# Kernel optimization log

Hardware: AMD Instinct MI355X
Metric: run time of the kernel (lower is better)

Reference implementation:

```python
import jax, jax.numpy as jnp
import numpy as np

K = 20.0          # wavenumber_k
L = 0.01          # grid_spacing_l
_lm = [L ** (i + 1) for i in range(7)]
C1 = jnp.array([[_lm[0], _lm[1]/2, _lm[2]/3, _lm[3]/4],
                [_lm[1]/2, _lm[2]/3, _lm[3]/4, _lm[4]/5],
                [_lm[2]/3, _lm[3]/4, _lm[4]/5, _lm[5]/6],
                [_lm[3]/4, _lm[4]/5, _lm[5]/6, _lm[6]/7]], dtype=jnp.float32)
C2 = jnp.array([[0,0,0,0],[0,0,0,0],[0,0,4*_lm[0],6*_lm[1]],[0,0,6*_lm[1],12*_lm[2]]], dtype=jnp.float32)
C3 = jnp.array([[0,0,0,0],[0,0,0,0],[2*_lm[0],_lm[1],2/3*_lm[2],1/2*_lm[3]],[3*_lm[1],2*_lm[2],3/2*_lm[3],6/5*_lm[4]]], dtype=jnp.float32)
M  = jnp.array([[1,0,0,0],[0,0,1,0],[-3/_lm[1],3/_lm[1],-2/_lm[0],-1/_lm[0]],[2/_lm[2],-2/_lm[2],1/_lm[1],1/_lm[1]]], dtype=jnp.float32)


def setup_inputs() -> dict:
    key = jax.random.key(0)
    x = jax.random.normal(key, (16, 4, 512, 512), dtype=jnp.float32)
    return {"x": x}


def _helmholtz(x):
    # corner views: (B, 4, H-1, W-1)
    tl = x[:, :, :-1, :-1]
    tr = x[:, :, :-1, 1:]
    bl = x[:, :, 1:, :-1]
    br = x[:, :, 1:, 1:]
    # rows replicate the original module exactly (including row_3's use of
    # du_xy_tl twice and du_x_tr); row_4 stacked on last dim.
    row1 = jnp.stack([tl[:, 0], tr[:, 0], tl[:, 2], tr[:, 2]], axis=-1)
    row2 = jnp.stack([bl[:, 0], br[:, 0], bl[:, 2], br[:, 2]], axis=-1)
    row3 = jnp.stack([tl[:, 3], tr[:, 1], tl[:, 3], tr[:, 3]], axis=-1)
    row4 = jnp.stack([bl[:, 1], br[:, 1], bl[:, 3], br[:, 3]], axis=-1)
    Q = jnp.stack([row1, row2, row3, row4], axis=-2)  # (B, H-1, W-1, 4, 4)
    # A = M @ Q @ M^T
    A = jnp.einsum('ij,bhwjk,lk->bhwil', M, Q, M)

    def quad(Cm):
        # sum over all entries of A @ Cm @ A^T, per patch -> (B, H-1, W-1)
        return jnp.einsum('bhwij,jk,bhwlk->bhw', A, Cm, A)

    s1 = jnp.sum(C1)
    s2 = jnp.sum(C2)
    s3 = jnp.sum(C3)
    qC1  = quad(C1)
    qC2  = quad(C2)
    qC3T = quad(C3.T)
    qC3  = quad(C3)
    k2 = K * K
    patch = (s2 * qC1 + s1 * qC2 + (k2 * k2) * s1 * qC1
             + 2.0 * s3 * qC3T + 2.0 * k2 * s1 * qC3 + 2.0 * k2 * s3 * qC1)
    return jnp.mean(patch)


def reference(x):
    return _helmholtz(x)
```

## Files before the change

kernel.cpp:

```cpp
#include <hip/hip_runtime.h>


struct HParams {
    float u0, u1, u2, u3;
    float H00, H11, H22, H33;
    float H01_2, H02_2, H03_2, H12_2, H13_2, H23_2;
};

#define BSIZE 256

__device__ __forceinline__ float f4get(const float4& v, int k) {
    switch (k & 3) { case 0: return v.x; case 1: return v.y; case 2: return v.z; default: return v.w; }
}

struct Fields { float f1[8], f2[8], f3[8], f4[8], f5[8]; };

#define LOADROW(B, r) do {                                                  \
    _Pragma("unroll")                                                       \
    for (int ch = 0; ch < 4; ++ch) {                                        \
        const size_t base_ = (size_t)ch * 65536u + (size_t)(r) * 128u + cq; \
        B[2*ch]   = px[base_];                                              \
        B[2*ch+1] = px[base_ + 1];                                          \
    } } while (0)

#define FIELDS(F, B) do {                                                   \
    _Pragma("unroll")                                                       \
    for (int j = 0; j < 8; ++j) {                                           \
        const float x0_ = f4get(B[0 + (j>>2)], j);                          \
        const float x1_ = f4get(B[2 + (j>>2)], j);                          \
        const float x2_ = f4get(B[4 + (j>>2)], j);                          \
        const float x3_ = f4get(B[6 + (j>>2)], j);                          \
        const float t0_ = P.u0 * x0_;                                       \
        F.f1[j] = fmaf(P.u2, x3_, t0_);                                     \
        F.f2[j] = fmaf(P.u2, x1_, t0_);                                     \
        F.f3[j] = fmaf(P.u3, x1_, P.u1 * x0_);                              \
        F.f4[j] = fmaf(P.u2, x3_, P.u0 * x2_);                              \
        F.f5[j] = fmaf(P.u3, x3_, P.u1 * x2_);                              \
    } } while (0)

#define PATCH(Ft, Fb) do {                                                  \
    float aV[8], bV[8], cV[8];                                              \
    _Pragma("unroll")                                                       \
    for (int j = 0; j < 8; ++j) {                                           \
        aV[j] = Ft.f1[j] + Fb.f3[j];                                        \
        bV[j] = Ft.f2[j] + Fb.f3[j];                                        \
        cV[j] = Ft.f4[j] + Fb.f5[j];                                        \
    }                                                                       \
    const float bn_ = __shfl_down(bV[0], 1, 64);                            \
    const float cn_ = __shfl_down(cV[0], 1, 64);                            \
    float rowsum_ = 0.0f;                                                   \
    _Pragma("unroll")                                                       \
    for (int j = 0; j < 8; ++j) {                                           \
        const float w0_ = aV[j];                                            \
        const float w1_ = (j < 7) ? bV[j+1] : bn_;                          \
        const float w2_ = cV[j];                                            \
        const float w3_ = (j < 7) ? cV[j+1] : cn_;                          \
        const float q0_ = fmaf(P.H03_2, w3_, fmaf(P.H02_2, w2_, fmaf(P.H01_2, w1_, P.H00 * w0_))); \
        const float q1_ = fmaf(P.H13_2, w3_, fmaf(P.H12_2, w2_, P.H11 * w1_)); \
        const float q2_ = fmaf(P.H23_2, w3_, P.H22 * w2_);                  \
        const float q3_ = P.H33 * w3_;                                      \
        const float pq_ = fmaf(w0_, q0_, fmaf(w1_, q1_, fmaf(w2_, q2_, w3_ * q3_))); \
        if (j < 7 || lane < 63) rowsum_ += pq_;                             \
    }                                                                       \
    acc += (double)rowsum_;                                                 \
} while (0)

__global__ __launch_bounds__(BSIZE) void helm_main(const float* __restrict__ x,
                                                   double* __restrict__ partial,
                                                   HParams P)
{
    const int t    = threadIdx.x;
    const int lane = t & 63;
    const int wid  = t >> 6;
    const int sid  = blockIdx.x * 4 + wid;
    const int b    = sid >> 6;
    const int tile = sid & 63;
    const int h0   = tile * 8;
    const int hend = min(h0 + 8, 511);

    const float4* px = (const float4*)(x + (size_t)b * (4u * 512u * 512u));
    const int cq = lane * 2;

    float4 A0[8], A1[8];
    Fields Fa, Fb;
    double acc = 0.0;

    LOADROW(A0, h0);
    LOADROW(A1, h0 + 1);
    FIELDS(Fa, A0);

    int r = h0 + 1;
    while (true) {
        if (r + 1 <= hend) LOADROW(A0, r + 1);
        FIELDS(Fb, A1);
        PATCH(Fa, Fb);
        ++r; if (r > hend) break;
        if (r + 1 <= hend) LOADROW(A1, r + 1);
        FIELDS(Fa, A0);
        PATCH(Fb, Fa);
        ++r; if (r > hend) break;
    }

    #pragma unroll
    for (int off = 32; off > 0; off >>= 1)
        acc += __shfl_down(acc, off, 64);
    if (lane == 0) partial[sid] = acc;
}

__global__ __launch_bounds__(BSIZE) void helm_reduce(const double* __restrict__ partial,
                                                     float* __restrict__ out, int n)
{
    __shared__ double wsum[4];
    const int t = threadIdx.x;
    double a = 0.0;
    for (int i = t; i < n; i += BSIZE) a += partial[i];
    #pragma unroll
    for (int off = 32; off > 0; off >>= 1)
        a += __shfl_down(a, off, 64);
    if ((t & 63) == 0) wsum[t >> 6] = a;
    __syncthreads();
    if (t == 0) {
        const double sum = wsum[0] + wsum[1] + wsum[2] + wsum[3];
        out[0] = (float)(sum / (16.0 * 511.0 * 511.0));
    }
}

extern "C" void kernel_launch(void* const* d_in, const int* in_sizes, int n_in,
                              void* d_out, int out_size, void* d_ws, size_t ws_size,
                              hipStream_t stream) {
    const float* x  = (const float*)d_in[0];
    float* out      = (float*)d_out;
    double* partial = (double*)d_ws;

    const double L = 0.01;
    double lm[7];
    lm[0] = L;
    for (int i = 1; i < 7; ++i) lm[i] = lm[i - 1] * L;

    double C1[4][4], C2[4][4] = {}, C3[4][4] = {};
    for (int i = 0; i < 4; ++i)
        for (int j = 0; j < 4; ++j)
            C1[i][j] = lm[i + j] / (double)(i + j + 1);
    C2[2][2] = 4.0 * lm[0];  C2[2][3] = 6.0 * lm[1];
    C2[3][2] = 6.0 * lm[1];  C2[3][3] = 12.0 * lm[2];
    C3[2][0] = 2.0 * lm[0];  C3[2][1] = lm[1];
    C3[2][2] = (2.0 / 3.0) * lm[2];  C3[2][3] = 0.5 * lm[3];
    C3[3][0] = 3.0 * lm[1];  C3[3][1] = 2.0 * lm[2];
    C3[3][2] = 1.5 * lm[3];  C3[3][3] = (6.0 / 5.0) * lm[4];

    const double M[4][4] = {
        {1.0, 0.0, 0.0, 0.0},
        {0.0, 0.0, 1.0, 0.0},
        {-3.0 / lm[1], 3.0 / lm[1], -2.0 / lm[0], -1.0 / lm[0]},
        { 2.0 / lm[2], -2.0 / lm[2], 1.0 / lm[1],  1.0 / lm[1]}
    };

    double s1 = 0.0, s2 = 0.0, s3 = 0.0;
    for (int i = 0; i < 4; ++i)
        for (int j = 0; j < 4; ++j) {
            s1 += C1[i][j]; s2 += C2[i][j]; s3 += C3[i][j];
        }

    const double k2 = 20.0 * 20.0;
    const double a1 = s2 + k2 * k2 * s1 + 2.0 * k2 * s3;
    const double a2 = s1;
    const double a3 = 2.0 * s3 + 2.0 * k2 * s1;

    double G[4][4];
    for (int i = 0; i < 4; ++i)
        for (int j = 0; j < 4; ++j)
            G[i][j] = a1 * C1[i][j] + a2 * C2[i][j] + a3 * C3[i][j];

    double H[4][4] = {};
    for (int jj = 0; jj < 4; ++jj)
        for (int kk = 0; kk < 4; ++kk) {
            double s = 0.0;
            for (int a = 0; a < 4; ++a)
                for (int bb = 0; bb < 4; ++bb)
                    s += M[a][jj] * G[a][bb] * M[bb][kk];
            H[jj][kk] = s;
        }
    double Hs[4][4];
    for (int i = 0; i < 4; ++i)
        for (int j = 0; j < 4; ++j)
            Hs[i][j] = 0.5 * (H[i][j] + H[j][i]);

    double u[4];
    for (int j = 0; j < 4; ++j)
        u[j] = M[0][j] + M[1][j] + M[2][j] + M[3][j];

    HParams P;
    P.u0 = (float)u[0]; P.u1 = (float)u[1]; P.u2 = (float)u[2]; P.u3 = (float)u[3];
    P.H00 = (float)Hs[0][0]; P.H11 = (float)Hs[1][1];
    P.H22 = (float)Hs[2][2]; P.H33 = (float)Hs[3][3];
    P.H01_2 = (float)(2.0 * Hs[0][1]); P.H02_2 = (float)(2.0 * Hs[0][2]);
    P.H03_2 = (float)(2.0 * Hs[0][3]); P.H12_2 = (float)(2.0 * Hs[1][2]);
    P.H13_2 = (float)(2.0 * Hs[1][3]); P.H23_2 = (float)(2.0 * Hs[2][3]);

    (void)in_sizes; (void)n_in; (void)out_size; (void)ws_size;

    helm_main<<<dim3(256), dim3(BSIZE), 0, stream>>>(x, partial, P);
    helm_reduce<<<dim3(1), dim3(BSIZE), 0, stream>>>(partial, out, 1024);
}
```

Before: 19.76 us.

## Split work into 4x finer tiles and fuse final reduction via last-block atomic

Each wave now handles 4 rows and one half of the columns (one float4 per channel per lane) instead of 8 rows and full width, so the grid grows from 256 to 1024 blocks to expose more parallelism on the many-CU GPU. The boundary column between halves is loaded separately by the edge lane. The separate reduce kernel is replaced by a last-block-done pattern using an atomic counter, with a memset launched before the kernel. This adds extra boundary loads, a memset, and atomics in exchange for better occupancy and one fewer kernel launch.

```diff
diff --git a/kernel.cpp b/kernel.cpp
--- a/kernel.cpp
+++ b/kernel.cpp
@@ -8,120 +8,147 @@
 };
 
 #define BSIZE 256
+#define NBLK  1024
 
 __device__ __forceinline__ float f4get(const float4& v, int k) {
     switch (k & 3) { case 0: return v.x; case 1: return v.y; case 2: return v.z; default: return v.w; }
 }
 
-struct Fields { float f1[8], f2[8], f3[8], f4[8], f5[8]; };
-
-#define LOADROW(B, r) do {                                                  \
-    _Pragma("unroll")                                                       \
-    for (int ch = 0; ch < 4; ++ch) {                                        \
-        const size_t base_ = (size_t)ch * 65536u + (size_t)(r) * 128u + cq; \
-        B[2*ch]   = px[base_];                                              \
-        B[2*ch+1] = px[base_ + 1];                                          \
+#define LOADROW(B, E, r) do {                                                     \
+    _Pragma("unroll")                                                             \
+    for (int ch = 0; ch < 4; ++ch)                                                \
+        B[ch] = pxf4[(size_t)ch * 65536u + (size_t)(r) * 128u + (size_t)cq];      \
+    if (ebnd) {                                                                   \
+        _Pragma("unroll")                                                         \
+        for (int ch = 0; ch < 4; ++ch)                                            \
+            E[ch] = pxf[(size_t)ch * 262144u + (size_t)(r) * 512u + 256u];        \
     } } while (0)
 
-#define FIELDS(F, B) do {                                                   \
-    _Pragma("unroll")                                                       \
-    for (int j = 0; j < 8; ++j) {                                           \
-        const float x0_ = f4get(B[0 + (j>>2)], j);                          \
-        const float x1_ = f4get(B[2 + (j>>2)], j);                          \
-        const float x2_ = f4get(B[4 + (j>>2)], j);                          \
-        const float x3_ = f4get(B[6 + (j>>2)], j);                          \
-        const float t0_ = P.u0 * x0_;                                       \
-        F.f1[j] = fmaf(P.u2, x3_, t0_);                                     \
-        F.f2[j] = fmaf(P.u2, x1_, t0_);                                     \
-        F.f3[j] = fmaf(P.u3, x1_, P.u1 * x0_);                              \
-        F.f4[j] = fmaf(P.u2, x3_, P.u0 * x2_);                              \
-        F.f5[j] = fmaf(P.u3, x3_, P.u1 * x2_);                              \
-    } } while (0)
-
-#define PATCH(Ft, Fb) do {                                                  \
-    float aV[8], bV[8], cV[8];                                              \
-    _Pragma("unroll")                                                       \
-    for (int j = 0; j < 8; ++j) {                                           \
-        aV[j] = Ft.f1[j] + Fb.f3[j];                                        \
-        bV[j] = Ft.f2[j] + Fb.f3[j];                                        \
-        cV[j] = Ft.f4[j] + Fb.f5[j];                                        \
-    }                                                                       \
-    const float bn_ = __shfl_down(bV[0], 1, 64);                            \
-    const float cn_ = __shfl_down(cV[0], 1, 64);                            \
-    float rowsum_ = 0.0f;                                                   \
-    _Pragma("unroll")                                                       \
-    for (int j = 0; j < 8; ++j) {                                           \
-        const float w0_ = aV[j];                                            \
-        const float w1_ = (j < 7) ? bV[j+1] : bn_;                          \
-        const float w2_ = cV[j];                                            \
-        const float w3_ = (j < 7) ? cV[j+1] : cn_;                          \
+#define TOPF(B, E) do {                                                           \
+    _Pragma("unroll")                                                             \
+    for (int j = 0; j < 4; ++j) {                                                 \
+        const float x0_ = f4get(B[0], j), x1_ = f4get(B[1], j);                   \
+        const float x2_ = f4get(B[2], j), x3_ = f4get(B[3], j);                   \
+        const float t0_ = P.u0 * x0_;                                             \
+        T1[j] = fmaf(P.u2, x3_, t0_);                                             \
+        T2[j] = fmaf(P.u2, x1_, t0_);                                             \
+        T4[j] = fmaf(P.u2, x3_, P.u0 * x2_);                                      \
+    }                                                                             \
+    Tb2 = fmaf(P.u2, E[1], P.u0 * E[0]);                                          \
+    Tb4 = fmaf(P.u2, E[3], P.u0 * E[2]);                                          \
+} while (0)
+
+#define ROWSTEP(B, E) do {                                                        \
+    float f3_[4], f5_[4];                                                         \
+    _Pragma("unroll")                                                             \
+    for (int j = 0; j < 4; ++j) {                                                 \
+        const float x0_ = f4get(B[0], j), x1_ = f4get(B[1], j);                   \
+        const float x2_ = f4get(B[2], j), x3_ = f4get(B[3], j);                   \
+        f3_[j] = fmaf(P.u3, x1_, P.u1 * x0_);                                     \
+        f5_[j] = fmaf(P.u3, x3_, P.u1 * x2_);                                     \
+    }                                                                             \
+    const float Bb3_ = fmaf(P.u3, E[1], P.u1 * E[0]);                             \
+    const float Bb5_ = fmaf(P.u3, E[3], P.u1 * E[2]);                             \
+    float aV[4], bV[4], cV[4];                                                    \
+    _Pragma("unroll")                                                             \
+    for (int j = 0; j < 4; ++j) {                                                 \
+        aV[j] = T1[j] + f3_[j];                                                   \
+        bV[j] = T2[j] + f3_[j];                                                   \
+        cV[j] = T4[j] + f5_[j];                                                   \
+    }                                                                             \
+    float bn_ = __shfl_down(bV[0], 1, 64);                                        \
+    float cn_ = __shfl_down(cV[0], 1, 64);                                        \
+    if (ebnd) { bn_ = Tb2 + Bb3_; cn_ = Tb4 + Bb5_; }                             \
+    float rowsum_ = 0.0f;                                                         \
+    _Pragma("unroll")                                                             \
+    for (int j = 0; j < 4; ++j) {                                                 \
+        const float w0_ = aV[j];                                                  \
+        const float w1_ = (j < 3) ? bV[j + 1] : bn_;                              \
+        const float w2_ = cV[j];                                                  \
+        const float w3_ = (j < 3) ? cV[j + 1] : cn_;                              \
         const float q0_ = fmaf(P.H03_2, w3_, fmaf(P.H02_2, w2_, fmaf(P.H01_2, w1_, P.H00 * w0_))); \
-        const float q1_ = fmaf(P.H13_2, w3_, fmaf(P.H12_2, w2_, P.H11 * w1_)); \
-        const float q2_ = fmaf(P.H23_2, w3_, P.H22 * w2_);                  \
-        const float q3_ = P.H33 * w3_;                                      \
+        const float q1_ = fmaf(P.H13_2, w3_, fmaf(P.H12_2, w2_, P.H11 * w1_));    \
+        const float q2_ = fmaf(P.H23_2, w3_, P.H22 * w2_);                        \
+        const float q3_ = P.H33 * w3_;                                            \
         const float pq_ = fmaf(w0_, q0_, fmaf(w1_, q1_, fmaf(w2_, q2_, w3_ * q3_))); \
-        if (j < 7 || lane < 63) rowsum_ += pq_;                             \
-    }                                                                       \
-    acc += (double)rowsum_;                                                 \
+        if (!(j == 3 && lane == 63 && half == 1)) rowsum_ += pq_;                 \
+    }                                                                             \
+    acc += (double)rowsum_;                                                       \
+    TOPF(B, E);                                                                   \
 } while (0)
 
-__global__ __launch_bounds__(BSIZE) void helm_main(const float* __restrict__ x,
-                                                   double* __restrict__ partial,
-                                                   HParams P)
+__global__ __launch_bounds__(BSIZE, 4) void helm_main(const float* __restrict__ x,
+                                                      double* __restrict__ partial,
+                                                      unsigned int* __restrict__ counter,
+                                                      float* __restrict__ out,
+                                                      HParams P)
 {
     const int t    = threadIdx.x;
     const int lane = t & 63;
     const int wid  = t >> 6;
     const int sid  = blockIdx.x * 4 + wid;
-    const int b    = sid >> 6;
-    const int tile = sid & 63;
-    const int h0   = tile * 8;
-    const int hend = min(h0 + 8, 511);
-
-    const float4* px = (const float4*)(x + (size_t)b * (4u * 512u * 512u));
-    const int cq = lane * 2;
-
-    float4 A0[8], A1[8];
-    Fields Fa, Fb;
+    const int b    = sid >> 8;
+    const int rem  = sid & 255;
+    const int half = rem & 1;
+    const int rs   = rem >> 1;
+    const int h0   = rs * 4;
+    const int hend = min(h0 + 4, 511);
+    const bool ebnd = (half == 0) && (lane == 63);
+
+    const float*  pxf  = x + (size_t)b * (4u * 512u * 512u);
+    const float4* pxf4 = (const float4*)pxf;
+    const int cq = half * 64 + lane;
+
+    float4 A0[4], A1[4];
+    float  E0[4] = {0.f, 0.f, 0.f, 0.f};
+    float  E1[4] = {0.f, 0.f, 0.f, 0.f};
+    float  T1[4], T2[4], T4[4];
+    float  Tb2 = 0.f, Tb4 = 0.f;
     double acc = 0.0;
 
-    LOADROW(A0, h0);
-    LOADROW(A1, h0 + 1);
-    FIELDS(Fa, A0);
+    LOADROW(A0, E0, h0);
+    LOADROW(A1, E1, h0 + 1);
+    TOPF(A0, E0);
 
     int r = h0 + 1;
     while (true) {
-        if (r + 1 <= hend) LOADROW(A0, r + 1);
-        FIELDS(Fb, A1);
-        PATCH(Fa, Fb);
+        if (r + 1 <= hend) LOADROW(A0, E0, r + 1);
+        ROWSTEP(A1, E1);
         ++r; if (r > hend) break;
-        if (r + 1 <= hend) LOADROW(A1, r + 1);
-        FIELDS(Fa, A0);
-        PATCH(Fb, Fa);
+        if (r + 1 <= hend) LOADROW(A1, E1, r + 1);
+        ROWSTEP(A0, E0);
         ++r; if (r > hend) break;
     }
 
+    __shared__ double wred[4];
+    __shared__ int    isLast;
     #pragma unroll
     for (int off = 32; off > 0; off >>= 1)
         acc += __shfl_down(acc, off, 64);
-    if (lane == 0) partial[sid] = acc;
-}
-
-__global__ __launch_bounds__(BSIZE) void helm_reduce(const double* __restrict__ partial,
-                                                     float* __restrict__ out, int n)
-{
-    __shared__ double wsum[4];
-    const int t = threadIdx.x;
-    double a = 0.0;
-    for (int i = t; i < n; i += BSIZE) a += partial[i];
-    #pragma unroll
-    for (int off = 32; off > 0; off >>= 1)
-        a += __shfl_down(a, off, 64);
-    if ((t & 63) == 0) wsum[t >> 6] = a;
+    if (lane == 0) wred[wid] = acc;
     __syncthreads();
     if (t == 0) {
-        const double sum = wsum[0] + wsum[1] + wsum[2] + wsum[3];
-        out[0] = (float)(sum / (16.0 * 511.0 * 511.0));
+        const double bsum = wred[0] + wred[1] + wred[2] + wred[3];
+        __hip_atomic_store(&partial[blockIdx.x], bsum, __ATOMIC_RELAXED, __HIP_MEMORY_SCOPE_AGENT);
+        const unsigned int old = __hip_atomic_fetch_add(counter, 1u, __ATOMIC_ACQ_REL, __HIP_MEMORY_SCOPE_AGENT);
+        isLast = (old == (unsigned int)(NBLK - 1)) ? 1 : 0;
+    }
+    __syncthreads();
+
+    if (isLast) {
+        double a = 0.0;
+        #pragma unroll
+        for (int k = 0; k < NBLK / BSIZE; ++k)
+            a += __hip_atomic_load(&partial[t + k * BSIZE], __ATOMIC_RELAXED, __HIP_MEMORY_SCOPE_AGENT);
+        #pragma unroll
+        for (int off = 32; off > 0; off >>= 1)
+            a += __shfl_down(a, off, 64);
+        if (lane == 0) wred[wid] = a;
+        __syncthreads();
+        if (t == 0) {
+            const double sum = wred[0] + wred[1] + wred[2] + wred[3];
+            out[0] = (float)(sum / (16.0 * 511.0 * 511.0));
+        }
     }
 }
 
@@ -131,6 +158,7 @@
     const float* x  = (const float*)d_in[0];
     float* out      = (float*)d_out;
     double* partial = (double*)d_ws;
+    unsigned int* counter = (unsigned int*)((char*)d_ws + NBLK * sizeof(double));
 
     const double L = 0.01;
     double lm[7];
@@ -199,6 +227,6 @@
 
     (void)in_sizes; (void)n_in; (void)out_size; (void)ws_size;
 
-    helm_main<<<dim3(256), dim3(BSIZE), 0, stream>>>(x, partial, P);
-    helm_reduce<<<dim3(1), dim3(BSIZE), 0, stream>>>(partial, out, 1024);
+    hipMemsetAsync(counter, 0, sizeof(unsigned int), stream);
+    helm_main<<<dim3(NBLK), dim3(BSIZE), 0, stream>>>(x, partial, counter, out, P);
 }
```

Result: slower. 52.06 us (+163.4%).
